# Optimization experiments

Measured on AMD Instinct MI355X. Metric: run time of the kernel, lower is better.

The kernel has to match this reference:

```python
import jax, jax.numpy as jnp
import numpy as np

N_NODES = 100000
N_EDGES = 1250000
IN_CH = 64
HID = 128
OUT_CH = 2
NUM_GRAPHS = 128


def setup_inputs() -> dict:
    key = jax.random.key(0)
    ks = jax.random.split(key, 6)
    x = jax.random.normal(ks[0], (N_NODES, IN_CH), dtype=jnp.float32)
    W_l = jax.random.normal(ks[1], (HID, IN_CH), dtype=jnp.float32) / np.sqrt(IN_CH)
    b_l = jnp.zeros((HID,), dtype=jnp.float32)
    W_r = jax.random.normal(ks[2], (HID, IN_CH), dtype=jnp.float32) / np.sqrt(IN_CH)
    W_lin = jax.random.normal(ks[3], (OUT_CH, HID), dtype=jnp.float32) / np.sqrt(HID)
    b_lin = jnp.zeros((OUT_CH,), dtype=jnp.float32)
    edge_index = jax.random.randint(ks[4], (2, N_EDGES), 0, N_NODES, dtype=jnp.int64)
    batch = jnp.sort(jax.random.randint(ks[5], (N_NODES,), 0, NUM_GRAPHS, dtype=jnp.int64))
    return {"x": x, "W_l": W_l, "b_l": b_l, "W_r": W_r, "W_lin": W_lin,
            "b_lin": b_lin, "edge_index": edge_index, "batch": batch}


def reference(x, W_l, b_l, W_r, W_lin, b_lin, edge_index, batch):
    src, dst = edge_index[0], edge_index[1]
    # SAGEConv (mean aggr): gather source features, scatter-sum to targets
    agg = jax.ops.segment_sum(x[src], dst, num_segments=N_NODES)          # [N, IN]
    cnt = jax.ops.segment_sum(jnp.ones((src.shape[0],), x.dtype), dst,
                              num_segments=N_NODES)                       # [N]
    mean = agg / jnp.maximum(cnt, 1.0)[:, None]
    h = jax.nn.relu(mean @ W_l.T + b_l + x @ W_r.T)                       # [N, HID]
    # global max pool per graph
    g = jax.ops.segment_max(h, batch, num_segments=NUM_GRAPHS)            # [G, HID]
    return g @ W_lin.T + b_lin                                            # [G, OUT]
```

## Files before the change

### kernel.cpp

```cpp
#include <hip/hip_runtime.h>
#include <hip/hip_fp8.h>

#define N_NODES 100000
#define N_EDGES 1250000
#define IN_CH 64
#define HID 128
#define OUT_CH 2
#define NUM_GRAPHS 128

#define PSHIFT 8
#define PSIZE 256
#define NPART ((N_NODES + PSIZE - 1) / PSIZE)
#define MAXE 4096
#define TILE 8192
#define PART_BLOCKS ((N_EDGES + TILE - 1) / TILE)

typedef _Float16 half2v __attribute__((ext_vector_type(2)));
typedef _Float16 half8 __attribute__((ext_vector_type(8)));
typedef float f32x4 __attribute__((ext_vector_type(4)));
typedef float f32x2 __attribute__((ext_vector_type(2)));

#define XCAST_BLOCKS (N_NODES * IN_CH / 4 / 512)
#define WPREP_BLOCKS 64
#define ZERO_BLOCKS 16
#define ZW_GMAX (NUM_GRAPHS * HID)
#define ZW_CUR 512
#define ZWORDS (ZW_GMAX + ZW_CUR)

__device__ __forceinline__ unsigned pkh2(float a, float b) {
    half2v h;
    h[0] = (_Float16)a;
    h[1] = (_Float16)b;
    return __builtin_bit_cast(unsigned, h);
}

__device__ __forceinline__ unsigned pk_fp8x4(float a, float b, float c, float d) {
#if __has_builtin(__builtin_amdgcn_cvt_pk_fp8_f32)
    int r = __builtin_amdgcn_cvt_pk_fp8_f32(a, b, 0, false);
    r = __builtin_amdgcn_cvt_pk_fp8_f32(c, d, r, true);
    return (unsigned)r;
#else
    __hip_fp8_e4m3 qa(a), qb(b), qc(c), qd(d);
    return (unsigned)qa.__x | ((unsigned)qb.__x << 8) | ((unsigned)qc.__x << 16) |
           ((unsigned)qd.__x << 24);
#endif
}

__device__ __forceinline__ void dec_fp8x4(float* a, unsigned u) {
#if __has_builtin(__builtin_amdgcn_cvt_pk_f32_fp8)
    const f32x2 lo = __builtin_amdgcn_cvt_pk_f32_fp8((int)u, false);
    const f32x2 hi = __builtin_amdgcn_cvt_pk_f32_fp8((int)u, true);
    a[0] += lo[0]; a[1] += lo[1]; a[2] += hi[0]; a[3] += hi[1];
#else
    __hip_fp8_e4m3 t0, t1, t2, t3;
    t0.__x = (unsigned char)u;
    t1.__x = (unsigned char)(u >> 8);
    t2.__x = (unsigned char)(u >> 16);
    t3.__x = (unsigned char)(u >> 24);
    a[0] += (float)t0; a[1] += (float)t1; a[2] += (float)t2; a[3] += (float)t3;
#endif
}

__device__ __forceinline__ void acc16p8(float* a, uint4 v) {
    dec_fp8x4(a + 0, v.x);
    dec_fp8x4(a + 4, v.y);
    dec_fp8x4(a + 8, v.z);
    dec_fp8x4(a + 12, v.w);
}

__global__ __launch_bounds__(256) void prep_k(const float* __restrict__ x,
                                              const float* __restrict__ W_l,
                                              const float* __restrict__ W_r,
                                              unsigned short* __restrict__ xh,
                                              unsigned char* __restrict__ xh8,
                                              unsigned short* __restrict__ Wc,
                                              unsigned* __restrict__ zbase) {
    const int b = (int)blockIdx.x;
    const int tid = (int)threadIdx.x;
    if (b < XCAST_BLOCKS) {
        const int u0 = (b * 256 + tid) * 2;
        const float4 v0 = reinterpret_cast<const float4*>(x)[u0];
        const float4 v1 = reinterpret_cast<const float4*>(x)[u0 + 1];
        uint4 hf;
        hf.x = pkh2(v0.x, v0.y);
        hf.y = pkh2(v0.z, v0.w);
        hf.z = pkh2(v1.x, v1.y);
        hf.w = pkh2(v1.z, v1.w);
        reinterpret_cast<uint4*>(xh)[u0 >> 1] = hf;
        uint2 q;
        q.x = pk_fp8x4(v0.x, v0.y, v0.z, v0.w);
        q.y = pk_fp8x4(v1.x, v1.y, v1.z, v1.w);
        reinterpret_cast<uint2*>(xh8)[u0 >> 1] = q;
        return;
    }
    const int b2 = b - XCAST_BLOCKS;
    if (b2 < WPREP_BLOCKS) {
        const int i = b2 * 256 + tid;
        if (i < HID * 2 * IN_CH) {
            const int o = i >> 7;
            const int k = i & 127;
            const float v = (k < IN_CH) ? W_l[o * IN_CH + k] : W_r[o * IN_CH + (k - IN_CH)];
            const _Float16 h = (_Float16)v;
            Wc[i] = __builtin_bit_cast(unsigned short, h);
        }
        return;
    }
    const int z = b2 - WPREP_BLOCKS;
    for (int i = z * 256 + tid; i < ZWORDS; i += ZERO_BLOCKS * 256) zbase[i] = 0u;
}

__global__ __launch_bounds__(512) void part_k(const int* __restrict__ ei,
                                              unsigned* __restrict__ gcursor,
                                              unsigned* __restrict__ edgesP) {
    __shared__ int lhist[512];
    __shared__ int lpre[512];
    __shared__ int gbase[512];
    __shared__ unsigned stage[TILE];
    __shared__ unsigned short sbin[TILE];
    __shared__ int sb[2][512];

    const int tid = (int)threadIdx.x;
    const int e0 = (int)blockIdx.x * TILE;
    const int nv = min(TILE, N_EDGES - e0);

    lhist[tid] = 0;
    __syncthreads();

    int esrc[16], emeta[16];
#pragma unroll
    for (int k = 0; k < 16; ++k) {
        const int e = e0 + k * 512 + tid;
        emeta[k] = -1;
        if (e < N_EDGES) {
            esrc[k] = ei[e];
            const int dst = ei[N_EDGES + e];
            const int bin = dst >> PSHIFT;
            const int dl = dst & (PSIZE - 1);
            const int rank = atomicAdd(&lhist[bin], 1);
            emeta[k] = bin | (dl << 9) | (rank << 17);
        }
    }
    __syncthreads();

    const int v = lhist[tid];
    sb[0][tid] = v;
    __syncthreads();
    int pb = 0;
    for (int o = 1; o < 512; o <<= 1) {
        sb[pb ^ 1][tid] = sb[pb][tid] + ((tid >= o) ? sb[pb][tid - o] : 0);
        pb ^= 1;
        __syncthreads();
    }
    lpre[tid] = sb[pb][tid] - v;
    if (tid < NPART) gbase[tid] = v ? (int)atomicAdd(&gcursor[tid], (unsigned)v) : 0;
    __syncthreads();

#pragma unroll
    for (int k = 0; k < 16; ++k) {
        if (emeta[k] >= 0) {
            const int bin = emeta[k] & 511;
            const int dl = (emeta[k] >> 9) & 255;
            const int rank = emeta[k] >> 17;
            const int pos = lpre[bin] + rank;
            stage[pos] = (unsigned)esrc[k] | ((unsigned)dl << 17);
            sbin[pos] = (unsigned short)bin;
        }
    }
    __syncthreads();

    for (int i = tid; i < nv; i += 512) {
        const int b = sbin[i];
        const int pos = gbase[b] + (i - lpre[b]);
        if (pos < MAXE) edgesP[(size_t)b * MAXE + pos] = stage[i];
    }
}

__global__ __launch_bounds__(512) void meanp_k(const unsigned char* __restrict__ xh8,
                                               const unsigned* __restrict__ gcursor,
                                               const unsigned* __restrict__ edgesP,
                                               unsigned short* __restrict__ meanh) {
    __shared__ int ss[MAXE];
    __shared__ unsigned char dl8[MAXE];
    __shared__ unsigned char rk8[MAXE];
    __shared__ int histL[PSIZE];
    __shared__ int rowp[PSIZE];
    __shared__ int sb[2][PSIZE];

    const int tid = (int)threadIdx.x;
    const int p = (int)blockIdx.x;
    const int node0 = p << PSHIFT;
    const size_t e0 = (size_t)p * MAXE;
    const int m = min((int)gcursor[p], MAXE);

    if (tid < PSIZE) histL[tid] = 0;
    __syncthreads();

    unsigned er[8];
    {
        int k = 0;
        for (int i = tid; i < m; i += 512, ++k) {
            const unsigned pr = edgesP[e0 + i];
            er[k] = pr;
            const int d = (int)((pr >> 17) & 255u);
            dl8[i] = (unsigned char)d;
            rk8[i] = (unsigned char)atomicAdd(&histL[d], 1);
        }
    }
    __syncthreads();

    if (tid < PSIZE) sb[0][tid] = histL[tid];
    __syncthreads();
    int pb = 0;
    for (int o = 1; o < PSIZE; o <<= 1) {
        if (tid < PSIZE)
            sb[pb ^ 1][tid] = sb[pb][tid] + ((tid >= o) ? sb[pb][tid - o] : 0);
        pb ^= 1;
        __syncthreads();
    }
    if (tid < PSIZE) rowp[tid] = sb[pb][tid] - histL[tid];
    __syncthreads();

    {
        int k = 0;
        for (int i = tid; i < m; i += 512, ++k)
            ss[rowp[dl8[i]] + rk8[i]] = (int)(er[k] & 0x1FFFFu);
    }
    __syncthreads();

    const int owner = tid >> 1;
    const int half = tid & 1;
    const int node = node0 + owner;
    if (node >= N_NODES) return;

    const int deg = histL[owner];
    const int base = rowp[owner];

    float acc[32];
#pragma unroll
    for (int i = 0; i < 32; ++i) acc[i] = 0.f;

    int j = 0;
    for (; j + 4 <= deg; j += 4) {
        const int s0 = ss[base + j];
        const int s1 = ss[base + j + 1];
        const int s2 = ss[base + j + 2];
        const int s3 = ss[base + j + 3];
        const uint4* r0 = reinterpret_cast<const uint4*>(xh8 + (size_t)s0 * IN_CH + half * 32);
        const uint4* r1 = reinterpret_cast<const uint4*>(xh8 + (size_t)s1 * IN_CH + half * 32);
        const uint4* r2 = reinterpret_cast<const uint4*>(xh8 + (size_t)s2 * IN_CH + half * 32);
        const uint4* r3 = reinterpret_cast<const uint4*>(xh8 + (size_t)s3 * IN_CH + half * 32);
        const uint4 a0 = r0[0], a1 = r0[1];
        const uint4 b0 = r1[0], b1 = r1[1];
        const uint4 c0 = r2[0], c1 = r2[1];
        const uint4 d0 = r3[0], d1 = r3[1];
        acc16p8(acc + 0, a0); acc16p8(acc + 16, a1);
        acc16p8(acc + 0, b0); acc16p8(acc + 16, b1);
        acc16p8(acc + 0, c0); acc16p8(acc + 16, c1);
        acc16p8(acc + 0, d0); acc16p8(acc + 16, d1);
    }
    for (; j < deg; ++j) {
        const int s0 = ss[base + j];
        const uint4* r0 = reinterpret_cast<const uint4*>(xh8 + (size_t)s0 * IN_CH + half * 32);
        const uint4 a0 = r0[0], a1 = r0[1];
        acc16p8(acc + 0, a0); acc16p8(acc + 16, a1);
    }

    const float rcp = 1.0f / fmaxf((float)deg, 1.0f);
    uint4 ov[4];
#pragma unroll
    for (int c = 0; c < 4; ++c) {
        ov[c].x = pkh2(acc[c * 8 + 0] * rcp, acc[c * 8 + 1] * rcp);
        ov[c].y = pkh2(acc[c * 8 + 2] * rcp, acc[c * 8 + 3] * rcp);
        ov[c].z = pkh2(acc[c * 8 + 4] * rcp, acc[c * 8 + 5] * rcp);
        ov[c].w = pkh2(acc[c * 8 + 6] * rcp, acc[c * 8 + 7] * rcp);
    }
    uint4* op = reinterpret_cast<uint4*>(meanh + (size_t)node * IN_CH + half * 32);
#pragma unroll
    for (int c = 0; c < 4; ++c) op[c] = ov[c];
}

#define MBLK 128

__device__ __forceinline__ void flushmax(unsigned* lmax, unsigned int* gmax,
                                         int g, int gbase, int l15,
                                         const float* rmax) {
    const int slot = g - gbase;
    if (slot < 4) {
#pragma unroll
        for (int nt = 0; nt < 8; ++nt)
            atomicMax(&lmax[slot * HID + nt * 16 + l15], __float_as_uint(rmax[nt]));
    } else {
#pragma unroll
        for (int nt = 0; nt < 8; ++nt)
            atomicMax(&gmax[(size_t)g * HID + nt * 16 + l15], __float_as_uint(rmax[nt]));
    }
}

__global__ __launch_bounds__(512) void gemm_pool_k(const unsigned short* __restrict__ xh,
                                                   const unsigned short* __restrict__ meanh,
                                                   const unsigned short* __restrict__ Wc,
                                                   const float* __restrict__ b_l,
                                                   const int* __restrict__ batch,
                                                   unsigned int* __restrict__ gmax) {
    __shared__ uint4 fe[MBLK * 16];
    __shared__ uint4 wt[HID * 16];
    __shared__ unsigned lmax[4 * HID];
    __shared__ int bt[MBLK];

    const int tid = (int)threadIdx.x;
    const int lane = tid & 63;
    const int w = tid >> 6;
    const int l15 = lane & 15, q = lane >> 4;

#pragma unroll
    for (int t = 0; t < 4; ++t) {
        const int id = tid + t * 512;
        const int row = id >> 4, c = id & 15;
        wt[row * 16 + (c ^ (row & 7))] = reinterpret_cast<const uint4*>(Wc)[row * 16 + c];
    }

    float bias[8];
#pragma unroll
    for (int nt = 0; nt < 8; ++nt) bias[nt] = b_l[nt * 16 + l15];

#pragma unroll 1
    for (int sub = 0; sub < 2; ++sub) {
        const int nb = (int)blockIdx.x * (2 * MBLK) + sub * MBLK;
        if (nb >= N_NODES) break;
        const int nvalid = min(MBLK, N_NODES - nb);

#pragma unroll
        for (int t = 0; t < 4; ++t) {
            const int id = tid + t * 512;
            const int row = id >> 4, c = id & 15;
            const int n = nb + row;
            uint4 v = make_uint4(0u, 0u, 0u, 0u);
            if (n < N_NODES) {
                v = (c < 8) ? reinterpret_cast<const uint4*>(meanh)[(size_t)n * 8 + c]
                            : reinterpret_cast<const uint4*>(xh)[(size_t)n * 8 + (c - 8)];
            }
            fe[row * 16 + (c ^ (row & 7))] = v;
        }
        if (tid < MBLK) bt[tid] = (nb + tid < N_NODES) ? batch[nb + tid] : -1;
        lmax[tid] = 0u;
        __syncthreads();

        f32x4 acc[8];
#pragma unroll
        for (int nt = 0; nt < 8; ++nt) acc[nt] = (f32x4){0.f, 0.f, 0.f, 0.f};

        const int arow = w * 16 + l15;
#pragma unroll
        for (int kb = 0; kb < 4; ++kb) {
            const int ac = kb * 4 + q;
            const half8 a = __builtin_bit_cast(half8, fe[arow * 16 + (ac ^ (arow & 7))]);
#pragma unroll
            for (int nt = 0; nt < 8; ++nt) {
                const int nrow = nt * 16 + l15;
                const half8 b = __builtin_bit_cast(half8, wt[nrow * 16 + (ac ^ (nrow & 7))]);
                acc[nt] = __builtin_amdgcn_mfma_f32_16x16x32_f16(a, b, acc[nt], 0, 0, 0);
            }
        }

        const int gbase = bt[0];
        const int rowb = w * 16 + q * 4;
        int curg = -1;
        float rmax[8];
#pragma unroll
        for (int nt = 0; nt < 8; ++nt) rmax[nt] = 0.f;

#pragma unroll
        for (int reg = 0; reg < 4; ++reg) {
            const int g = bt[rowb + reg];
            if (g >= 0) {
                float h[8];
#pragma unroll
                for (int nt = 0; nt < 8; ++nt) h[nt] = fmaxf(acc[nt][reg] + bias[nt], 0.f);
                if (g != curg) {
                    if (curg >= 0) flushmax(lmax, gmax, curg, gbase, l15, rmax);
                    curg = g;
#pragma unroll
                    for (int nt = 0; nt < 8; ++nt) rmax[nt] = h[nt];
                } else {
#pragma unroll
                    for (int nt = 0; nt < 8; ++nt) rmax[nt] = fmaxf(rmax[nt], h[nt]);
                }
            }
        }
        if (curg >= 0) flushmax(lmax, gmax, curg, gbase, l15, rmax);
        __syncthreads();

        int span = bt[nvalid - 1] - gbase + 1;
        if (span > 4) span = 4;
        if (tid < span * HID) {
            const unsigned v = lmax[tid];
            if (v) atomicMax(&gmax[(size_t)(gbase + (tid >> 7)) * HID + (tid & 127)], v);
        }
        __syncthreads();
    }
}

__global__ __launch_bounds__(256) void head_k(const unsigned int* __restrict__ gmax_u,
                                              const float* __restrict__ W_lin,
                                              const float* __restrict__ b_lin,
                                              float* __restrict__ out) {
    const int t = (int)threadIdx.x;
    const int g = t >> 1;
    const int oc = t & 1;
    const float4* gr = reinterpret_cast<const float4*>((const float*)gmax_u + (size_t)g * HID);
    const float4* wr = reinterpret_cast<const float4*>(W_lin + oc * HID);
    float acc = b_lin[oc];
#pragma unroll 8
    for (int k = 0; k < HID / 4; ++k) {
        const float4 a = gr[k];
        const float4 w = wr[k];
        acc += a.x * w.x + a.y * w.y + a.z * w.z + a.w * w.w;
    }
    out[(size_t)g * OUT_CH + oc] = acc;
}

extern "C" void kernel_launch(void* const* d_in, const int* in_sizes, int n_in,
                              void* d_out, int out_size, void* d_ws, size_t ws_size,
                              hipStream_t stream) {
    const float* x = (const float*)d_in[0];
    const float* W_l = (const float*)d_in[1];
    const float* b_l = (const float*)d_in[2];
    const float* W_r = (const float*)d_in[3];
    const float* W_lin = (const float*)d_in[4];
    const float* b_lin = (const float*)d_in[5];
    const int* ei = (const int*)d_in[6];
    const int* batch = (const int*)d_in[7];
    float* out = (float*)d_out;

    char* ws = (char*)d_ws;
    size_t o = 0;
    unsigned* zbase = (unsigned*)(ws + o);
    unsigned int* gmax = zbase;
    unsigned* gcursor = zbase + ZW_GMAX;
    o += (size_t)ZWORDS * 4;
    o = (o + 255) & ~(size_t)255;
    unsigned* edgesP = (unsigned*)(ws + o); o += (size_t)NPART * MAXE * 4;
    unsigned short* xh = (unsigned short*)(ws + o); o += (size_t)N_NODES * IN_CH * 2;
    unsigned char* xh8 = (unsigned char*)(ws + o); o += (size_t)N_NODES * IN_CH;
    unsigned short* meanh = (unsigned short*)(ws + o); o += (size_t)N_NODES * IN_CH * 2;
    unsigned short* Wc = (unsigned short*)(ws + o); o += (size_t)HID * 2 * IN_CH * 2;


    prep_k<<<XCAST_BLOCKS + WPREP_BLOCKS + ZERO_BLOCKS, 256, 0, stream>>>(
        x, W_l, W_r, xh, xh8, Wc, zbase);
    part_k<<<PART_BLOCKS, 512, 0, stream>>>(ei, gcursor, edgesP);
    meanp_k<<<NPART, 512, 0, stream>>>(xh8, gcursor, edgesP, meanh);
    gemm_pool_k<<<(N_NODES + 2 * MBLK - 1) / (2 * MBLK), 512, 0, stream>>>(
        xh, meanh, Wc, b_l, batch, gmax);
    head_k<<<1, 256, 0, stream>>>(gmax, W_lin, b_lin, out);
}
```

Before: 68.97 us.

## Use direct global-to-LDS loads for GEMM tiles and wave-shuffle prefix scan

The partition kernel's 512-entry block prefix scan changes from a double-buffered shared-memory Hillis-Steele loop with many barriers to a wave-level shuffle scan plus a small cross-wave combine. In the GEMM kernel, the weight tile and full feature tiles are loaded with global_load_lds 16-byte direct-to-LDS transfers, with the XOR swizzle applied on the source address side, which avoids staging through VGPRs. Partial tail tiles keep the old path. A risk is that the direct LDS loads may need explicit waits (vmcnt) before the barrier, and this relies on the 16-byte global_load_lds support available on gfx950.

```diff
diff --git a/kernel.cpp b/kernel.cpp
--- a/kernel.cpp
+++ b/kernel.cpp
@@ -19,6 +19,9 @@
 typedef _Float16 half8 __attribute__((ext_vector_type(8)));
 typedef float f32x4 __attribute__((ext_vector_type(4)));
 typedef float f32x2 __attribute__((ext_vector_type(2)));
+
+#define AS1 __attribute__((address_space(1)))
+#define AS3 __attribute__((address_space(3)))
 
 #define XCAST_BLOCKS (N_NODES * IN_CH / 4 / 512)
 #define WPREP_BLOCKS 64
@@ -117,9 +120,11 @@
     __shared__ int gbase[512];
     __shared__ unsigned stage[TILE];
     __shared__ unsigned short sbin[TILE];
-    __shared__ int sb[2][512];
+    __shared__ int wsum[8], wpre[8];
 
     const int tid = (int)threadIdx.x;
+    const int lane = tid & 63;
+    const int wv = tid >> 6;
     const int e0 = (int)blockIdx.x * TILE;
     const int nv = min(TILE, N_EDGES - e0);
 
@@ -143,15 +148,26 @@
     __syncthreads();
 
     const int v = lhist[tid];
-    sb[0][tid] = v;
-    __syncthreads();
-    int pb = 0;
-    for (int o = 1; o < 512; o <<= 1) {
-        sb[pb ^ 1][tid] = sb[pb][tid] + ((tid >= o) ? sb[pb][tid - o] : 0);
-        pb ^= 1;
-        __syncthreads();
-    }
-    lpre[tid] = sb[pb][tid] - v;
+    int s = v;
+#pragma unroll
+    for (int o = 1; o < 64; o <<= 1) {
+        const int t = __shfl_up(s, o, 64);
+        if (lane >= o) s += t;
+    }
+    if (lane == 63) wsum[wv] = s;
+    __syncthreads();
+    if (wv == 0) {
+        const int ws = (lane < 8) ? wsum[lane] : 0;
+        int p = ws;
+#pragma unroll
+        for (int o = 1; o < 8; o <<= 1) {
+            const int t = __shfl_up(p, o, 64);
+            if (lane >= o) p += t;
+        }
+        if (lane < 8) wpre[lane] = p - ws;
+    }
+    __syncthreads();
+    lpre[tid] = (s - v) + wpre[wv];
     if (tid < NPART) gbase[tid] = v ? (int)atomicAdd(&gcursor[tid], (unsigned)v) : 0;
     __syncthreads();
 
@@ -315,8 +331,11 @@
 #pragma unroll
     for (int t = 0; t < 4; ++t) {
         const int id = tid + t * 512;
-        const int row = id >> 4, c = id & 15;
-        wt[row * 16 + (c ^ (row & 7))] = reinterpret_cast<const uint4*>(Wc)[row * 16 + c];
+        const int row = id >> 4, cs = id & 15;
+        const int c = cs ^ (row & 7);
+        __builtin_amdgcn_global_load_lds(
+            (const AS1 unsigned*)(reinterpret_cast<const uint4*>(Wc) + (row * 16 + c)),
+            (AS3 unsigned*)&wt[w * 64 + t * 512], 16, 0, 0);
     }
 
     float bias[8];
@@ -329,17 +348,33 @@
         if (nb >= N_NODES) break;
         const int nvalid = min(MBLK, N_NODES - nb);
 
-#pragma unroll
-        for (int t = 0; t < 4; ++t) {
-            const int id = tid + t * 512;
-            const int row = id >> 4, c = id & 15;
-            const int n = nb + row;
-            uint4 v = make_uint4(0u, 0u, 0u, 0u);
-            if (n < N_NODES) {
-                v = (c < 8) ? reinterpret_cast<const uint4*>(meanh)[(size_t)n * 8 + c]
-                            : reinterpret_cast<const uint4*>(xh)[(size_t)n * 8 + (c - 8)];
+        if (nvalid == MBLK) {
+#pragma unroll
+            for (int t = 0; t < 4; ++t) {
+                const int id = tid + t * 512;
+                const int row = id >> 4, cs = id & 15;
+                const int c = cs ^ (row & 7);
+                const int n = nb + row;
+                const uint4* src = (c < 8)
+                    ? (reinterpret_cast<const uint4*>(meanh) + ((size_t)n * 8 + c))
+                    : (reinterpret_cast<const uint4*>(xh) + ((size_t)n * 8 + (c - 8)));
+                __builtin_amdgcn_global_load_lds(
+                    (const AS1 unsigned*)src,
+                    (AS3 unsigned*)&fe[w * 64 + t * 512], 16, 0, 0);
             }
-            fe[row * 16 + (c ^ (row & 7))] = v;
+        } else {
+#pragma unroll
+            for (int t = 0; t < 4; ++t) {
+                const int id = tid + t * 512;
+                const int row = id >> 4, c = id & 15;
+                const int n = nb + row;
+                uint4 v = make_uint4(0u, 0u, 0u, 0u);
+                if (n < N_NODES) {
+                    v = (c < 8) ? reinterpret_cast<const uint4*>(meanh)[(size_t)n * 8 + c]
+                                : reinterpret_cast<const uint4*>(xh)[(size_t)n * 8 + (c - 8)];
+                }
+                fe[row * 16 + (c ^ (row & 7))] = v;
+            }
         }
         if (tid < MBLK) bt[tid] = (nb + tid < N_NODES) ? batch[nb + tid] : -1;
         lmax[tid] = 0u;
```

After: 66.96 us (median of 2 runs). 1.03x faster.
